# Performance work log

Hardware: AMD Instinct MI355X
Metric: run time of the kernel (lower is better)

The kernel has to match this reference:

```python
import jax, jax.numpy as jnp
import numpy as np

QUERY_DIM = 1024
KEY_DIM = 1024
NUM_HEADS = 16
HEAD_DIM = QUERY_DIM // NUM_HEADS


def setup_inputs() -> dict:
    key = jax.random.key(0)
    ks = jax.random.split(key, 11)
    B, Sq, Sk = 2, 2048, 2048
    s = 0.02
    return {
        "q": jax.random.normal(ks[0], (B, Sq, QUERY_DIM), jnp.float32),
        "k": jax.random.normal(ks[1], (B, Sk, KEY_DIM), jnp.float32),
        "v": jax.random.normal(ks[2], (B, Sk, KEY_DIM), jnp.float32),
        "Wq": jax.random.normal(ks[3], (QUERY_DIM, QUERY_DIM), jnp.float32) * s,
        "bq": jnp.zeros((QUERY_DIM,), jnp.float32),
        "Wk": jax.random.normal(ks[4], (KEY_DIM, QUERY_DIM), jnp.float32) * s,
        "bk": jnp.zeros((QUERY_DIM,), jnp.float32),
        "Wv": jax.random.normal(ks[5], (KEY_DIM, QUERY_DIM), jnp.float32) * s,
        "bv": jnp.zeros((QUERY_DIM,), jnp.float32),
        "Wo": jax.random.normal(ks[6], (QUERY_DIM, QUERY_DIM), jnp.float32) * s,
        "bo": jnp.zeros((QUERY_DIM,), jnp.float32),
    }


def reference(q, k, v, Wq, bq, Wk, bk, Wv, bv, Wo, bo):
    B, Sq, _ = q.shape
    Sk = k.shape[1]
    scale = HEAD_DIM ** -0.5
    # projections -> [B, H, S, Dh]
    qh = (q @ Wq + bq).reshape(B, Sq, NUM_HEADS, HEAD_DIM).transpose(0, 2, 1, 3)
    kh = (k @ Wk + bk).reshape(B, Sk, NUM_HEADS, HEAD_DIM).transpose(0, 2, 1, 3)
    vh = (v @ Wv + bv).reshape(B, Sk, NUM_HEADS, HEAD_DIM).transpose(0, 2, 1, 3)
    scores = jnp.einsum("bhqd,bhkd->bhqk", qh, kh) * scale
    attn = jax.nn.softmax(scores, axis=-1)
    out = jnp.einsum("bhqk,bhkd->bhqd", attn, vh)
    out = out.transpose(0, 2, 1, 3).reshape(B, Sq, QUERY_DIM)
    return out @ Wo + bo  # dropout is identity at inference
```

## Files before the change

### kernel.cpp

```cpp
#include <hip/hip_runtime.h>
#include <hip/hip_fp16.h>
#include <cstddef>


#define B_   2
#define S_   2048
#define D_   1024
#define H_   16
#define DH_  64

typedef _Float16 half8 __attribute__((ext_vector_type(8)));
typedef _Float16 half4 __attribute__((ext_vector_type(4)));
typedef float floatx4 __attribute__((ext_vector_type(4)));

#define MFMA16(a, b, c) __builtin_amdgcn_mfma_f32_16x16x32_f16((a), (b), (c), 0, 0, 0)

__global__ __launch_bounds__(256) void cvt3(
    const float* __restrict__ q, const float* __restrict__ k,
    const float* __restrict__ v,
    __half* __restrict__ qf, __half* __restrict__ kf, __half* __restrict__ vf)
{
    const float* srcs[3] = {q, k, v};
    __half* dsts[3] = {qf, kf, vf};
    const int z = blockIdx.y;
    const int i = blockIdx.x * 256 + threadIdx.x;
    const float4* s = (const float4*)srcs[z];
    const float4 a = s[2 * i], b = s[2 * i + 1];
    half8 h;
    h[0] = (_Float16)a.x; h[1] = (_Float16)a.y; h[2] = (_Float16)a.z; h[3] = (_Float16)a.w;
    h[4] = (_Float16)b.x; h[5] = (_Float16)b.y; h[6] = (_Float16)b.z; h[7] = (_Float16)b.w;
    *(half8*)&dsts[z][(size_t)i * 8] = h;
}

__global__ __launch_bounds__(256) void wtrans4(
    const float* __restrict__ Wq, const float* __restrict__ Wk,
    const float* __restrict__ Wv, const float* __restrict__ Wo,
    __half* __restrict__ Wtq, __half* __restrict__ Wtk,
    __half* __restrict__ Wtv, __half* __restrict__ Wto)
{
    __shared__ __align__(16) __half T[64][72];
    const float* Ws[4] = {Wq, Wk, Wv, Wo};
    __half* Wts[4] = {Wtq, Wtk, Wtv, Wto};
    const float* W = Ws[blockIdx.z];
    __half* Wt = Wts[blockIdx.z];
    const int tid = threadIdx.x;
    const int n0 = blockIdx.x * 64, k0 = blockIdx.y * 64;
    #pragma unroll
    for (int p = 0; p < 4; ++p) {
        const int c = tid + p * 256;
        const int kr = c >> 4, nc = (c & 15) * 4;
        const float4 a = *(const float4*)&W[(size_t)(k0 + kr) * D_ + n0 + nc];
        T[nc + 0][kr] = __float2half(a.x);
        T[nc + 1][kr] = __float2half(a.y);
        T[nc + 2][kr] = __float2half(a.z);
        T[nc + 3][kr] = __float2half(a.w);
    }
    __syncthreads();
    #pragma unroll
    for (int p = 0; p < 2; ++p) {
        const int c = tid + p * 256;
        const int nr = c >> 3, kc = (c & 7) * 8;
        *(half8*)&Wt[(size_t)(n0 + nr) * D_ + k0 + kc] = *(const half8*)&T[nr][kc];
    }
}

__device__ __forceinline__ void gemm_core(
    const __half* __restrict__ A, const __half* __restrict__ Bt,
    const float* __restrict__ bias, void* __restrict__ dst,
    const int mode, const float oscale)
{
    __shared__ __align__(16) __half As[128][72];
    __shared__ __align__(16) __half Bs[128][72];

    const int tid = threadIdx.x;
    const int m0 = blockIdx.y * 128, n0 = blockIdx.x * 128;
    const int lane = tid & 63, wv = tid >> 6;
    const int quad = lane >> 4, lr = lane & 15;
    const int wm0 = (wv >> 1) * 64, wn0 = (wv & 1) * 64;

    floatx4 acc[4][4];
    #pragma unroll
    for (int i = 0; i < 4; ++i)
        #pragma unroll
        for (int j = 0; j < 4; ++j)
            acc[i][j] = (floatx4){0.f, 0.f, 0.f, 0.f};

    const int srow = tid >> 3;
    (void)srow;
    for (int k0 = 0; k0 < D_; k0 += 64) {
        __syncthreads();
        #pragma unroll
        for (int p = 0; p < 4; ++p) {
            const int c = tid + p * 256;
            const int row = c >> 3, seg = (c & 7) * 8;
            *(half8*)&As[row][seg] = *(const half8*)&A [(size_t)(m0 + row) * D_ + k0 + seg];
            *(half8*)&Bs[row][seg] = *(const half8*)&Bt[(size_t)(n0 + row) * D_ + k0 + seg];
        }
        __syncthreads();
        #pragma unroll
        for (int ks = 0; ks < 2; ++ks) {
            const int ko = quad * 8 + ks * 32;
            half8 af[4], bf[4];
            #pragma unroll
            for (int i = 0; i < 4; ++i) af[i] = *(const half8*)&As[wm0 + i * 16 + lr][ko];
            #pragma unroll
            for (int j = 0; j < 4; ++j) bf[j] = *(const half8*)&Bs[wn0 + j * 16 + lr][ko];
            #pragma unroll
            for (int i = 0; i < 4; ++i)
                #pragma unroll
                for (int j = 0; j < 4; ++j)
                    acc[i][j] = MFMA16(af[i], bf[j], acc[i][j]);
        }
    }

    #pragma unroll
    for (int i = 0; i < 4; ++i) {
        #pragma unroll
        for (int j = 0; j < 4; ++j) {
            const int col = n0 + wn0 + j * 16 + lr;
            const float bval = bias[col];
            if (mode == 1) {
                float* out = (float*)dst;
                #pragma unroll
                for (int r = 0; r < 4; ++r) {
                    const int m = m0 + wm0 + i * 16 + quad * 4 + r;
                    out[(size_t)m * D_ + col] = acc[i][j][r] + bval;
                }
            } else if (mode == 0) {
                __half* oh = (__half*)dst;
                const int h = col >> 6, d = col & 63;
                #pragma unroll
                for (int r = 0; r < 4; ++r) {
                    const int m = m0 + wm0 + i * 16 + quad * 4 + r;
                    const int b = m >> 11, s = m & (S_ - 1);
                    oh[(((size_t)(b * H_ + h) * S_ + s) << 6) + d] =
                        __float2half((acc[i][j][r] + bval) * oscale);
                }
            } else {
                __half* oh = (__half*)dst;
                const int h = col >> 6, d = col & 63;
                const int mb = m0 + wm0 + i * 16 + quad * 4;
                const int b = mb >> 11, s0 = mb & (S_ - 1);
                half4 pk;
                #pragma unroll
                for (int r = 0; r < 4; ++r)
                    pk[r] = (_Float16)(acc[i][j][r] + bval);
                *(half4*)&oh[((size_t)(b * H_ + h) * DH_ + d) * S_ + s0] = pk;
            }
        }
    }
}

__global__ __launch_bounds__(256) void gemm_proj(
    const __half* __restrict__ qf, const __half* __restrict__ kf,
    const __half* __restrict__ vf,
    const __half* __restrict__ Wtq, const __half* __restrict__ Wtk,
    const __half* __restrict__ Wtv,
    const float* __restrict__ bq, const float* __restrict__ bk,
    const float* __restrict__ bv,
    __half* __restrict__ qhf, __half* __restrict__ khf, __half* __restrict__ vht)
{
    const __half* As[3] = {qf, kf, vf};
    const __half* Bts[3] = {Wtq, Wtk, Wtv};
    const float* bs[3] = {bq, bk, bv};
    __half* ds[3] = {qhf, khf, vht};
    const int z = blockIdx.z;
    gemm_core(As[z], Bts[z], bs[z], ds[z], z == 2 ? 2 : 0, z == 0 ? 0.125f : 1.0f);
}

__global__ __launch_bounds__(256) void gemm_final(
    const __half* __restrict__ attf, const __half* __restrict__ Wto,
    const float* __restrict__ bo, float* __restrict__ out)
{
    gemm_core(attf, Wto, bo, out, 1, 1.0f);
}

__global__ __launch_bounds__(256) void attn_f16(
    const __half* __restrict__ qhf, const __half* __restrict__ khf,
    const __half* __restrict__ vht, __half* __restrict__ attf)
{
    __shared__ __align__(16) __half Qs[64][72];
    __shared__ __align__(16) __half Ks[64][72];
    __shared__ __align__(16) __half Vs[64][72];
    __shared__ __align__(16) __half Ps[64][68];

    const int tid = threadIdx.x;
    const int lane = tid & 63, wv = tid >> 6;
    const int quad = lane >> 4, lr = lane & 15;
    const int bh = blockIdx.y;
    const int q0 = blockIdx.x * 64;
    const size_t hbase = (size_t)bh * S_ * DH_;

    #pragma unroll
    for (int p = 0; p < 2; ++p) {
        const int c = tid + p * 256;
        const int row = c >> 3, seg = (c & 7) * 8;
        *(half8*)&Qs[row][seg] = *(const half8*)&qhf[hbase + (size_t)(q0 + row) * DH_ + seg];
    }

    float lp[4] = {0.f, 0.f, 0.f, 0.f};
    floatx4 O[4] = {{0.f,0.f,0.f,0.f},{0.f,0.f,0.f,0.f},
                    {0.f,0.f,0.f,0.f},{0.f,0.f,0.f,0.f}};

    for (int kt = 0; kt < S_; kt += 64) {
        __syncthreads();
        #pragma unroll
        for (int p = 0; p < 2; ++p) {
            const int c = tid + p * 256;
            const int row = c >> 3, seg = (c & 7) * 8;
            *(half8*)&Ks[row][seg] = *(const half8*)&khf[hbase + (size_t)(kt + row) * DH_ + seg];
            *(half8*)&Vs[row][seg] = *(const half8*)&vht[hbase + (size_t)row * S_ + kt + seg];
        }
        __syncthreads();

        floatx4 s4[4] = {{0.f,0.f,0.f,0.f},{0.f,0.f,0.f,0.f},
                         {0.f,0.f,0.f,0.f},{0.f,0.f,0.f,0.f}};
        #pragma unroll
        for (int ks = 0; ks < 2; ++ks) {
            const int ko = quad * 8 + ks * 32;
            const half8 aq = *(const half8*)&Qs[wv * 16 + lr][ko];
            #pragma unroll
            for (int in = 0; in < 4; ++in) {
                const half8 bk = *(const half8*)&Ks[in * 16 + lr][ko];
                s4[in] = MFMA16(aq, bk, s4[in]);
            }
        }

        #pragma unroll
        for (int in = 0; in < 4; ++in) {
            #pragma unroll
            for (int r = 0; r < 4; ++r) {
                const float p = __expf(s4[in][r]);
                lp[r] += p;
                Ps[wv * 16 + quad * 4 + r][in * 16 + lr] = __float2half(p);
            }
        }
        __syncthreads();

        #pragma unroll
        for (int ks = 0; ks < 2; ++ks) {
            const int ko = quad * 8 + ks * 32;
            const half8 ap = *(const half8*)&Ps[wv * 16 + lr][ko];
            #pragma unroll
            for (int in = 0; in < 4; ++in) {
                const half8 bv = *(const half8*)&Vs[in * 16 + lr][ko];
                O[in] = MFMA16(ap, bv, O[in]);
            }
        }
    }

    float inv[4];
    #pragma unroll
    for (int r = 0; r < 4; ++r) {
        float rs = lp[r];
        rs += __shfl_xor(rs, 1);
        rs += __shfl_xor(rs, 2);
        rs += __shfl_xor(rs, 4);
        rs += __shfl_xor(rs, 8);
        inv[r] = 1.0f / rs;
    }
    const int b = bh >> 4, h = bh & 15;
    #pragma unroll
    for (int in = 0; in < 4; ++in) {
        const int d = in * 16 + lr;
        #pragma unroll
        for (int r = 0; r < 4; ++r) {
            const int q = q0 + wv * 16 + quad * 4 + r;
            attf[((size_t)(b * S_ + q) << 10) + h * DH_ + d] =
                __float2half(O[in][r] * inv[r]);
        }
    }
}

extern "C" void kernel_launch(void* const* d_in, const int* in_sizes, int n_in,
                              void* d_out, int out_size, void* d_ws, size_t ws_size,
                              hipStream_t stream) {
    const float* q  = (const float*)d_in[0];
    const float* k  = (const float*)d_in[1];
    const float* v  = (const float*)d_in[2];
    const float* Wq = (const float*)d_in[3];
    const float* bq = (const float*)d_in[4];
    const float* Wk = (const float*)d_in[5];
    const float* bk = (const float*)d_in[6];
    const float* Wv = (const float*)d_in[7];
    const float* bv = (const float*)d_in[8];
    const float* Wo = (const float*)d_in[9];
    const float* bo = (const float*)d_in[10];
    float* out = (float*)d_out;

    __half* ws = (__half*)d_ws;
    const size_t NE = (size_t)B_ * S_ * D_;
    __half* qf   = ws;
    __half* kf   = ws + NE;
    __half* vf   = ws + 2 * NE;
    __half* qhf  = ws + 3 * NE;
    __half* khf  = ws + 4 * NE;
    __half* vht  = ws + 5 * NE;
    __half* attf = ws + 6 * NE;
    __half* Wtq  = ws + 7 * NE;
    __half* Wtk  = Wtq + (size_t)D_ * D_;
    __half* Wtv  = Wtk + (size_t)D_ * D_;
    __half* Wto  = Wtv + (size_t)D_ * D_;

    const dim3 blk(256);
    cvt3<<<dim3((unsigned)(NE / 8 / 256), 3), blk, 0, stream>>>(q, k, v, qf, kf, vf);
    wtrans4<<<dim3(16, 16, 4), blk, 0, stream>>>(Wq, Wk, Wv, Wo, Wtq, Wtk, Wtv, Wto);

    gemm_proj<<<dim3(D_ / 128, (B_ * S_) / 128, 3), blk, 0, stream>>>(
        qf, kf, vf, Wtq, Wtk, Wtv, bq, bk, bv, qhf, khf, vht);

    attn_f16<<<dim3(S_ / 64, B_ * H_), blk, 0, stream>>>(qhf, khf, vht, attf);

    gemm_final<<<dim3(D_ / 128, (B_ * S_) / 128), blk, 0, stream>>>(attf, Wto, bo, out);
}
```

Measured before the change: 269.3 us.

## Fuse fp32-to-half conversion into projection GEMM and restructure attention kernel

Removes the separate cvt3 pass by converting the fp32 q/k/v activations to half inside the projection GEMM's tile load. The projection epilogue now stages results through shared memory so it can write vectorised half8 stores in the head-split and transposed layouts. The attention kernel is restructured: Q fragments are kept in registers, S is computed with K as the A operand so P stays in registers and feeds a 16x16x16 MFMA against V without a shared-memory round trip or the extra barrier. Each wave accumulates over a 16-key slice, which needs a cross-wave reduction of O and of the row sums through shared memory at the end. In exchange, the fp32 A tile loads in the GEMM double global read bytes per tile, and attention holds more accumulator registers.

After: 288.7 us. +7.2%, slower.

```diff
diff --git a/kernel.cpp b/kernel.cpp
--- a/kernel.cpp
+++ b/kernel.cpp
@@ -13,24 +13,8 @@
 typedef _Float16 half4 __attribute__((ext_vector_type(4)));
 typedef float floatx4 __attribute__((ext_vector_type(4)));
 
-#define MFMA16(a, b, c) __builtin_amdgcn_mfma_f32_16x16x32_f16((a), (b), (c), 0, 0, 0)
-
-__global__ __launch_bounds__(256) void cvt3(
-    const float* __restrict__ q, const float* __restrict__ k,
-    const float* __restrict__ v,
-    __half* __restrict__ qf, __half* __restrict__ kf, __half* __restrict__ vf)
-{
-    const float* srcs[3] = {q, k, v};
-    __half* dsts[3] = {qf, kf, vf};
-    const int z = blockIdx.y;
-    const int i = blockIdx.x * 256 + threadIdx.x;
-    const float4* s = (const float4*)srcs[z];
-    const float4 a = s[2 * i], b = s[2 * i + 1];
-    half8 h;
-    h[0] = (_Float16)a.x; h[1] = (_Float16)a.y; h[2] = (_Float16)a.z; h[3] = (_Float16)a.w;
-    h[4] = (_Float16)b.x; h[5] = (_Float16)b.y; h[6] = (_Float16)b.z; h[7] = (_Float16)b.w;
-    *(half8*)&dsts[z][(size_t)i * 8] = h;
-}
+#define MFMA32(a, b, c) __builtin_amdgcn_mfma_f32_16x16x32_f16((a), (b), (c), 0, 0, 0)
+#define MFMA16(a, b, c) __builtin_amdgcn_mfma_f32_16x16x16f16((a), (b), (c), 0, 0, 0)
 
 __global__ __launch_bounds__(256) void wtrans4(
     const float* __restrict__ Wq, const float* __restrict__ Wk,
@@ -64,13 +48,15 @@
     }
 }
 
+template<bool AF32>
 __device__ __forceinline__ void gemm_core(
-    const __half* __restrict__ A, const __half* __restrict__ Bt,
+    const void* __restrict__ A_, const __half* __restrict__ Bt,
     const float* __restrict__ bias, void* __restrict__ dst,
     const int mode, const float oscale)
 {
-    __shared__ __align__(16) __half As[128][72];
-    __shared__ __align__(16) __half Bs[128][72];
+    __shared__ __align__(16) char gsm[36864];
+    __half (*As)[72] = (__half(*)[72])gsm;
+    __half (*Bs)[72] = (__half(*)[72])(gsm + 18432);
 
     const int tid = threadIdx.x;
     const int m0 = blockIdx.y * 128, n0 = blockIdx.x * 128;
@@ -78,6 +64,9 @@
     const int quad = lane >> 4, lr = lane & 15;
     const int wm0 = (wv >> 1) * 64, wn0 = (wv & 1) * 64;
 
+    const float* A32 = (const float*)A_;
+    const __half* A16 = (const __half*)A_;
+
     floatx4 acc[4][4];
     #pragma unroll
     for (int i = 0; i < 4; ++i)
@@ -85,15 +74,24 @@
         for (int j = 0; j < 4; ++j)
             acc[i][j] = (floatx4){0.f, 0.f, 0.f, 0.f};
 
-    const int srow = tid >> 3;
-    (void)srow;
     for (int k0 = 0; k0 < D_; k0 += 64) {
         __syncthreads();
         #pragma unroll
         for (int p = 0; p < 4; ++p) {
             const int c = tid + p * 256;
             const int row = c >> 3, seg = (c & 7) * 8;
-            *(half8*)&As[row][seg] = *(const half8*)&A [(size_t)(m0 + row) * D_ + k0 + seg];
+            if (AF32) {
+                const float4 f0 = *(const float4*)&A32[(size_t)(m0 + row) * D_ + k0 + seg];
+                const float4 f1 = *(const float4*)&A32[(size_t)(m0 + row) * D_ + k0 + seg + 4];
+                half8 h;
+                h[0] = (_Float16)f0.x; h[1] = (_Float16)f0.y;
+                h[2] = (_Float16)f0.z; h[3] = (_Float16)f0.w;
+                h[4] = (_Float16)f1.x; h[5] = (_Float16)f1.y;
+                h[6] = (_Float16)f1.z; h[7] = (_Float16)f1.w;
+                *(half8*)&As[row][seg] = h;
+            } else {
+                *(half8*)&As[row][seg] = *(const half8*)&A16[(size_t)(m0 + row) * D_ + k0 + seg];
+            }
             *(half8*)&Bs[row][seg] = *(const half8*)&Bt[(size_t)(n0 + row) * D_ + k0 + seg];
         }
         __syncthreads();
@@ -109,80 +107,98 @@
             for (int i = 0; i < 4; ++i)
                 #pragma unroll
                 for (int j = 0; j < 4; ++j)
-                    acc[i][j] = MFMA16(af[i], bf[j], acc[i][j]);
-        }
-    }
-
-    #pragma unroll
-    for (int i = 0; i < 4; ++i) {
-        #pragma unroll
-        for (int j = 0; j < 4; ++j) {
-            const int col = n0 + wn0 + j * 16 + lr;
-            const float bval = bias[col];
-            if (mode == 1) {
-                float* out = (float*)dst;
+                    acc[i][j] = MFMA32(af[i], bf[j], acc[i][j]);
+        }
+    }
+
+    if (mode == 1) {
+        float* out = (float*)dst;
+        #pragma unroll
+        for (int i = 0; i < 4; ++i) {
+            #pragma unroll
+            for (int j = 0; j < 4; ++j) {
+                const int col = n0 + wn0 + j * 16 + lr;
+                const float bval = bias[col];
                 #pragma unroll
                 for (int r = 0; r < 4; ++r) {
                     const int m = m0 + wm0 + i * 16 + quad * 4 + r;
                     out[(size_t)m * D_ + col] = acc[i][j][r] + bval;
                 }
-            } else if (mode == 0) {
-                __half* oh = (__half*)dst;
-                const int h = col >> 6, d = col & 63;
-                #pragma unroll
-                for (int r = 0; r < 4; ++r) {
-                    const int m = m0 + wm0 + i * 16 + quad * 4 + r;
-                    const int b = m >> 11, s = m & (S_ - 1);
-                    oh[(((size_t)(b * H_ + h) * S_ + s) << 6) + d] =
-                        __float2half((acc[i][j][r] + bval) * oscale);
-                }
-            } else {
-                __half* oh = (__half*)dst;
-                const int h = col >> 6, d = col & 63;
-                const int mb = m0 + wm0 + i * 16 + quad * 4;
-                const int b = mb >> 11, s0 = mb & (S_ - 1);
-                half4 pk;
-                #pragma unroll
-                for (int r = 0; r < 4; ++r)
-                    pk[r] = (_Float16)(acc[i][j][r] + bval);
-                *(half4*)&oh[((size_t)(b * H_ + h) * DH_ + d) * S_ + s0] = pk;
             }
         }
+        return;
+    }
+
+    __syncthreads();
+    __half (*Ct)[136] = (__half(*)[136])gsm;
+    #pragma unroll
+    for (int i = 0; i < 4; ++i) {
+        #pragma unroll
+        for (int j = 0; j < 4; ++j) {
+            const int nl = wn0 + j * 16 + lr;
+            const float bval = bias[n0 + nl];
+            #pragma unroll
+            for (int r = 0; r < 4; ++r) {
+                const int ml = wm0 + i * 16 + quad * 4 + r;
+                const _Float16 hv = (_Float16)((acc[i][j][r] + bval) * oscale);
+                if (mode == 0) Ct[ml][nl] = hv;
+                else           Ct[nl][ml] = hv;
+            }
+        }
+    }
+    __syncthreads();
+    __half* oh = (__half*)dst;
+    #pragma unroll
+    for (int p = 0; p < 8; ++p) {
+        const int row = (tid >> 4) + p * 16;
+        const int cs  = (tid & 15) * 8;
+        const half8 vls = *(const half8*)&Ct[row][cs];
+        if (mode == 0) {
+            const int m = m0 + row, col = n0 + cs;
+            const int b = m >> 11, s = m & (S_ - 1);
+            const int h = col >> 6, d = col & 63;
+            *(half8*)&oh[(((size_t)(b * H_ + h) * S_ + s) << 6) + d] = vls;
+        } else {
+            const int col = n0 + row, m = m0 + cs;
+            const int b = m >> 11, s = m & (S_ - 1);
+            const int h = col >> 6, d = col & 63;
+            *(half8*)&oh[((size_t)(b * H_ + h) * DH_ + d) * S_ + s] = vls;
+        }
     }
 }
 
 __global__ __launch_bounds__(256) void gemm_proj(
-    const __half* __restrict__ qf, const __half* __restrict__ kf,
-    const __half* __restrict__ vf,
+    const float* __restrict__ q, const float* __restrict__ k,
+    const float* __restrict__ v,
     const __half* __restrict__ Wtq, const __half* __restrict__ Wtk,
     const __half* __restrict__ Wtv,
     const float* __restrict__ bq, const float* __restrict__ bk,
     const float* __restrict__ bv,
     __half* __restrict__ qhf, __half* __restrict__ khf, __half* __restrict__ vht)
 {
-    const __half* As[3] = {qf, kf, vf};
+    const void* As[3] = {q, k, v};
     const __half* Bts[3] = {Wtq, Wtk, Wtv};
     const float* bs[3] = {bq, bk, bv};
     __half* ds[3] = {qhf, khf, vht};
     const int z = blockIdx.z;
-    gemm_core(As[z], Bts[z], bs[z], ds[z], z == 2 ? 2 : 0, z == 0 ? 0.125f : 1.0f);
+    gemm_core<true>(As[z], Bts[z], bs[z], ds[z], z == 2 ? 2 : 0, z == 0 ? 0.125f : 1.0f);
 }
 
 __global__ __launch_bounds__(256) void gemm_final(
     const __half* __restrict__ attf, const __half* __restrict__ Wto,
     const float* __restrict__ bo, float* __restrict__ out)
 {
-    gemm_core(attf, Wto, bo, out, 1, 1.0f);
+    gemm_core<false>(attf, Wto, bo, out, 1, 1.0f);
 }
 
 __global__ __launch_bounds__(256) void attn_f16(
     const __half* __restrict__ qhf, const __half* __restrict__ khf,
     const __half* __restrict__ vht, __half* __restrict__ attf)
 {
-    __shared__ __align__(16) __half Qs[64][72];
-    __shared__ __align__(16) __half Ks[64][72];
-    __shared__ __align__(16) __half Vs[64][72];
-    __shared__ __align__(16) __half Ps[64][68];
+    __shared__ __align__(16) char smem[31232];
+    __half (*Qs)[72] = (__half(*)[72])smem;
+    __half (*Ks)[72] = (__half(*)[72])(smem + 9216);
+    __half (*Vs)[72] = (__half(*)[72])(smem + 18432);
 
     const int tid = threadIdx.x;
     const int lane = tid & 63, wv = tid >> 6;
@@ -197,10 +213,21 @@
         const int row = c >> 3, seg = (c & 7) * 8;
         *(half8*)&Qs[row][seg] = *(const half8*)&qhf[hbase + (size_t)(q0 + row) * DH_ + seg];
     }
+    __syncthreads();
+    half8 qB[4][2];
+    #pragma unroll
+    for (int qs = 0; qs < 4; ++qs)
+        #pragma unroll
+        for (int ks = 0; ks < 2; ++ks)
+            qB[qs][ks] = *(const half8*)&Qs[qs * 16 + lr][quad * 8 + ks * 32];
 
     float lp[4] = {0.f, 0.f, 0.f, 0.f};
-    floatx4 O[4] = {{0.f,0.f,0.f,0.f},{0.f,0.f,0.f,0.f},
-                    {0.f,0.f,0.f,0.f},{0.f,0.f,0.f,0.f}};
+    floatx4 O[4][4];
+    #pragma unroll
+    for (int i = 0; i < 4; ++i)
+        #pragma unroll
+        for (int j = 0; j < 4; ++j)
+            O[i][j] = (floatx4){0.f, 0.f, 0.f, 0.f};
 
     for (int kt = 0; kt < S_; kt += 64) {
         __syncthreads();
@@ -213,63 +240,83 @@
         }
         __syncthreads();
 
-        floatx4 s4[4] = {{0.f,0.f,0.f,0.f},{0.f,0.f,0.f,0.f},
-                         {0.f,0.f,0.f,0.f},{0.f,0.f,0.f,0.f}};
+        floatx4 s4[4];
+        #pragma unroll
+        for (int qs = 0; qs < 4; ++qs) s4[qs] = (floatx4){0.f, 0.f, 0.f, 0.f};
         #pragma unroll
         for (int ks = 0; ks < 2; ++ks) {
-            const int ko = quad * 8 + ks * 32;
-            const half8 aq = *(const half8*)&Qs[wv * 16 + lr][ko];
-            #pragma unroll
-            for (int in = 0; in < 4; ++in) {
-                const half8 bk = *(const half8*)&Ks[in * 16 + lr][ko];
-                s4[in] = MFMA16(aq, bk, s4[in]);
+            const half8 aK = *(const half8*)&Ks[wv * 16 + lr][quad * 8 + ks * 32];
+            #pragma unroll
+            for (int qs = 0; qs < 4; ++qs)
+                s4[qs] = MFMA32(aK, qB[qs][ks], s4[qs]);
+        }
+
+        half4 pB[4];
+        #pragma unroll
+        for (int qs = 0; qs < 4; ++qs) {
+            #pragma unroll
+            for (int r = 0; r < 4; ++r) {
+                const float p = __expf(s4[qs][r]);
+                lp[qs] += p;
+                pB[qs][r] = (_Float16)p;
             }
         }
 
         #pragma unroll
-        for (int in = 0; in < 4; ++in) {
-            #pragma unroll
-            for (int r = 0; r < 4; ++r) {
-                const float p = __expf(s4[in][r]);
-                lp[r] += p;
-                Ps[wv * 16 + quad * 4 + r][in * 16 + lr] = __float2half(p);
-            }
-        }
-        __syncthreads();
-
-        #pragma unroll
-        for (int ks = 0; ks < 2; ++ks) {
-            const int ko = quad * 8 + ks * 32;
-            const half8 ap = *(const half8*)&Ps[wv * 16 + lr][ko];
-            #pragma unroll
-            for (int in = 0; in < 4; ++in) {
-                const half8 bv = *(const half8*)&Vs[in * 16 + lr][ko];
-                O[in] = MFMA16(ap, bv, O[in]);
-            }
-        }
-    }
-
-    float inv[4];
-    #pragma unroll
-    for (int r = 0; r < 4; ++r) {
-        float rs = lp[r];
-        rs += __shfl_xor(rs, 1);
-        rs += __shfl_xor(rs, 2);
-        rs += __shfl_xor(rs, 4);
-        rs += __shfl_xor(rs, 8);
-        inv[r] = 1.0f / rs;
-    }
+        for (int ds = 0; ds < 4; ++ds) {
+            const half4 aV = *(const half4*)&Vs[ds * 16 + lr][wv * 16 + quad * 4];
+            #pragma unroll
+            for (int qs = 0; qs < 4; ++qs)
+                O[ds][qs] = MFMA16(aV, pB[qs], O[ds][qs]);
+        }
+    }
+
+    __syncthreads();
+    float* L    = (float*)(smem + 17408);
+    float* invL = (float*)(smem + 21504);
+    float (*R)[68] = (float(*)[68])smem;
+    __half (*F)[72] = (__half(*)[72])(smem + 22016);
+
+    #pragma unroll
+    for (int qs = 0; qs < 4; ++qs)
+        L[(wv * 4 + quad) * 64 + qs * 16 + lr] = lp[qs];
+    __syncthreads();
+    if (tid < 64) {
+        float s = 0.f;
+        #pragma unroll
+        for (int i = 0; i < 16; ++i) s += L[i * 64 + tid];
+        invL[tid] = 1.0f / s;
+    }
+    __syncthreads();
+
+    const int qc = tid & 63, dg = tid >> 6;
+    const float il = invL[qc];
+
+    #pragma unroll
+    for (int ds = 0; ds < 4; ++ds) {
+        __syncthreads();
+        #pragma unroll
+        for (int qs = 0; qs < 4; ++qs)
+            #pragma unroll
+            for (int r = 0; r < 4; ++r)
+                R[wv * 16 + quad * 4 + r][qs * 16 + lr] = O[ds][qs][r];
+        __syncthreads();
+        half4 hv;
+        #pragma unroll
+        for (int rr = 0; rr < 4; ++rr) {
+            const int row = dg * 4 + rr;
+            const float v = R[row][qc] + R[16 + row][qc] + R[32 + row][qc] + R[48 + row][qc];
+            hv[rr] = (_Float16)(v * il);
+        }
+        *(half4*)&F[qc][ds * 16 + dg * 4] = hv;
+    }
+    __syncthreads();
+
     const int b = bh >> 4, h = bh & 15;
-    #pragma unroll
-    for (int in = 0; in < 4; ++in) {
-        const int d = in * 16 + lr;
-        #pragma unroll
-        for (int r = 0; r < 4; ++r) {
-            const int q = q0 + wv * 16 + quad * 4 + r;
-            attf[((size_t)(b * S_ + q) << 10) + h * DH_ + d] =
-                __float2half(O[in][r] * inv[r]);
-        }
-    }
+    const int qrow = tid >> 2, dseg = (tid & 3) * 16;
+    __half* dstp = &attf[(((size_t)(b * S_ + q0 + qrow)) << 10) + h * DH_ + dseg];
+    *(half8*)&dstp[0] = *(const half8*)&F[qrow][dseg];
+    *(half8*)&dstp[8] = *(const half8*)&F[qrow][dseg + 8];
 }
 
 extern "C" void kernel_launch(void* const* d_in, const int* in_sizes, int n_in,
@@ -290,24 +337,20 @@
 
     __half* ws = (__half*)d_ws;
     const size_t NE = (size_t)B_ * S_ * D_;
-    __half* qf   = ws;
-    __half* kf   = ws + NE;
-    __half* vf   = ws + 2 * NE;
-    __half* qhf  = ws + 3 * NE;
-    __half* khf  = ws + 4 * NE;
-    __half* vht  = ws + 5 * NE;
-    __half* attf = ws + 6 * NE;
-    __half* Wtq  = ws + 7 * NE;
+    __half* qhf  = ws;
+    __half* khf  = ws + NE;
+    __half* vht  = ws + 2 * NE;
+    __half* attf = ws + 3 * NE;
+    __half* Wtq  = ws + 4 * NE;
     __half* Wtk  = Wtq + (size_t)D_ * D_;
     __half* Wtv  = Wtk + (size_t)D_ * D_;
     __half* Wto  = Wtv + (size_t)D_ * D_;
 
     const dim3 blk(256);
-    cvt3<<<dim3((unsigned)(NE / 8 / 256), 3), blk, 0, stream>>>(q, k, v, qf, kf, vf);
     wtrans4<<<dim3(16, 16, 4), blk, 0, stream>>>(Wq, Wk, Wv, Wo, Wtq, Wtk, Wtv, Wto);
 
     gemm_proj<<<dim3(D_ / 128, (B_ * S_) / 128, 3), blk, 0, stream>>>(
-        qf, kf, vf, Wtq, Wtk, Wtv, bq, bk, bv, qhf, khf, vht);
+        q, k, v, Wtq, Wtk, Wtv, bq, bk, bv, qhf, khf, vht);
 
     attn_f16<<<dim3(S_ / 64, B_ * H_), blk, 0, stream>>>(qhf, khf, vht, attf);
 
```
